# Optimization experiments

Hardware: AMD Instinct MI355X
Metric: run time of the kernel (lower is better)

The kernel has to match this reference:

```python
import jax, jax.numpy as jnp
import numpy as np

N_NODES = 100000


def _deg_norm(idx, n):
    # inverse-sqrt degree, zero-degree nodes -> 0 (DGL norm='both' convention)
    deg = jax.ops.segment_sum(jnp.ones(idx.shape, jnp.float32), idx, num_segments=n)
    return jnp.where(deg > 0, jax.lax.rsqrt(jnp.maximum(deg, 1.0)), 0.0)


def graph_conv(x, src, dst, W, b, n):
    # symmetric normalization: D_out^{-1/2} on src, D_in^{-1/2} on dst
    norm_src = _deg_norm(src, n)  # [N]
    norm_dst = _deg_norm(dst, n)  # [N]
    h = (x * norm_src[:, None]) @ W          # apply weight first (in >= out)
    msg = h[src]                              # gather [E, out]
    agg = jax.ops.segment_sum(msg, dst, num_segments=n)  # scatter-add [N, out]
    return agg * norm_dst[:, None] + b


def setup_inputs() -> dict:
    key = jax.random.key(0)
    ks = jax.random.split(key, 6)
    x = jax.random.normal(ks[0], (N_NODES, 128), dtype=jnp.float32)
    edge_index = jax.random.randint(ks[1], (2, 1600000), 0, N_NODES, dtype=jnp.int64)
    W1 = jax.random.normal(ks[2], (128, 64), dtype=jnp.float32) * (1.0 / np.sqrt(128))
    b1 = jnp.zeros((64,), jnp.float32)
    W2 = jax.random.normal(ks[3], (64, 32), dtype=jnp.float32) * (1.0 / np.sqrt(64))
    b2 = jnp.zeros((32,), jnp.float32)
    Wl = jax.random.normal(ks[4], (32, 1), dtype=jnp.float32) * (1.0 / np.sqrt(32))
    bl = jnp.zeros((1,), jnp.float32)
    return {"x": x, "edge_index": edge_index, "W1": W1, "b1": b1,
            "W2": W2, "b2": b2, "Wl": Wl, "bl": bl}


def reference(x, edge_index, W1, b1, W2, b2, Wl, bl):
    src, dst = edge_index[0], edge_index[1]
    n = x.shape[0]
    h = graph_conv(x, src, dst, W1, b1, n)
    h = jax.nn.relu(h)
    # dropout(p=0.5) is identity at inference
    h = graph_conv(h, src, dst, W2, b2, n)
    return h @ Wl + bl  # [N, 1]
```

## Files before the change

kernel.cpp:

```cpp
#include <hip/hip_runtime.h>
#include <hip/hip_fp16.h>


#define WAVE 64
#define NRANGE 8

typedef _Float16 f16x8 __attribute__((ext_vector_type(8)));
typedef float f32x4 __attribute__((ext_vector_type(4)));

__global__ __launch_bounds__(256) void k_hist(const int* __restrict__ srcArr,
                                              const int* __restrict__ dstArr,
                                              unsigned* __restrict__ partial_s,
                                              unsigned* __restrict__ partial_d,
                                              int E, int B, int C, int chunkE) {
    extern __shared__ unsigned hist[];
    const int r = blockIdx.x & (NRANGE - 1);
    const int c = blockIdx.x >> 3;
    const int lo = r * B;
    const int* nodes = blockIdx.y ? dstArr : srcArr;
    unsigned* partial = blockIdx.y ? partial_d : partial_s;

    for (int b = threadIdx.x; b < B; b += 256) hist[b] = 0u;
    __syncthreads();

    const int beg = c * chunkE, end = min(beg + chunkE, E);
    const int n4 = (end - beg) >> 2;
    const int4* p = (const int4*)(nodes + beg);
    for (int j = threadIdx.x; j < n4; j += 256) {
        int4 v = p[j];
        int a;
        a = v.x - lo; if ((unsigned)a < (unsigned)B) atomicAdd(&hist[a], 1u);
        a = v.y - lo; if ((unsigned)a < (unsigned)B) atomicAdd(&hist[a], 1u);
        a = v.z - lo; if ((unsigned)a < (unsigned)B) atomicAdd(&hist[a], 1u);
        a = v.w - lo; if ((unsigned)a < (unsigned)B) atomicAdd(&hist[a], 1u);
    }
    for (int j = beg + (n4 << 2) + threadIdx.x; j < end; j += 256) {
        int a = nodes[j] - lo;
        if ((unsigned)a < (unsigned)B) atomicAdd(&hist[a], 1u);
    }
    __syncthreads();
    unsigned* outp = partial + (size_t)(r * C + c) * B;
    for (int b = threadIdx.x; b < B; b += 256) outp[b] = hist[b];
}

__global__ __launch_bounds__(256) void k_reduce_norm(const unsigned* __restrict__ partial_s,
                                                     unsigned* __restrict__ partial_d,
                                                     float* __restrict__ norm_s,
                                                     float* __restrict__ norm_d,
                                                     unsigned* __restrict__ deg_d,
                                                     int N, int B, int C) {
    int i = blockIdx.x * 256 + threadIdx.x;
    if (i >= N) return;
    int r = i / B, b = i - r * B;
    size_t base = (size_t)r * C * B + b;
    unsigned ds = 0;
    for (int c = 0; c < C; ++c) ds += partial_s[base + (size_t)c * B];
    unsigned dd = 0;
    for (int c = 0; c < C; ++c) {
        size_t ix = base + (size_t)c * B;
        unsigned v = partial_d[ix];
        partial_d[ix] = dd;
        dd += v;
    }
    deg_d[i] = dd;
    norm_s[i] = ds ? rsqrtf((float)ds) : 0.0f;
    norm_d[i] = dd ? rsqrtf((float)dd) : 0.0f;
}

__global__ void k_w2l(const float* __restrict__ W2, const float* __restrict__ b2,
                      const float* __restrict__ Wl, const float* __restrict__ bl,
                      float* __restrict__ w2l, float* __restrict__ c0) {
    int c = threadIdx.x;
    float acc = 0.f;
#pragma unroll
    for (int j = 0; j < 32; ++j) acc += W2[c * 32 + j] * Wl[j];
    w2l[c] = acc;
    if (c == 0) {
        float s = 0.f;
#pragma unroll
        for (int j = 0; j < 32; ++j) s += b2[j] * Wl[j];
        *c0 = s + bl[0];
    }
}

__global__ __launch_bounds__(256) void k_wt(const float* __restrict__ W1,
                                            _Float16* __restrict__ wt) {
    int t = threadIdx.x;
    for (int i = 0; i < 32; ++i) {
        int e = i * 256 + t;
        int k = e >> 6, n = e & 63;
        wt[n * 128 + k] = (_Float16)W1[e];
    }
}

__global__ __launch_bounds__(256) void k_blocksum(const unsigned* __restrict__ deg,
                                                  unsigned* __restrict__ partial, int N) {
    __shared__ unsigned sw[4];
    int i = blockIdx.x * 256 + threadIdx.x;
    unsigned v = (i < N) ? deg[i] : 0u;
#pragma unroll
    for (int off = 32; off; off >>= 1) v += __shfl_xor((int)v, off);
    if ((threadIdx.x & 63) == 0) sw[threadIdx.x >> 6] = v;
    __syncthreads();
    if (threadIdx.x == 0) partial[blockIdx.x] = sw[0] + sw[1] + sw[2] + sw[3];
}

__global__ __launch_bounds__(512) void k_scanpartial(const unsigned* __restrict__ partial,
                                                     unsigned* __restrict__ blockoff,
                                                     unsigned* __restrict__ offsets,
                                                     int nb, int N) {
    __shared__ unsigned s[512];
    int t = threadIdx.x;
    unsigned v = (t < nb) ? partial[t] : 0u;
    s[t] = v;
    __syncthreads();
    for (int off = 1; off < 512; off <<= 1) {
        unsigned a = (t >= off) ? s[t - off] : 0u;
        __syncthreads();
        s[t] += a;
        __syncthreads();
    }
    if (t < nb) blockoff[t] = s[t] - v;
    if (t == nb - 1) offsets[N] = s[t];
}

__global__ __launch_bounds__(256) void k_offsets(const unsigned* __restrict__ deg,
                                                 const unsigned* __restrict__ blockoff,
                                                 unsigned* __restrict__ offsets, int N) {
    __shared__ unsigned s[256];
    int t = threadIdx.x;
    int i = blockIdx.x * 256 + t;
    unsigned v = (i < N) ? deg[i] : 0u;
    s[t] = v;
    __syncthreads();
    for (int off = 1; off < 256; off <<= 1) {
        unsigned a = (t >= off) ? s[t - off] : 0u;
        __syncthreads();
        s[t] += a;
        __syncthreads();
    }
    if (i < N) offsets[i] = blockoff[blockIdx.x] + s[t] - v;
}

__global__ __launch_bounds__(256) void k_fill(const int* __restrict__ src,
                                              const int* __restrict__ dst,
                                              const unsigned* __restrict__ offsets,
                                              const unsigned* __restrict__ rel,
                                              unsigned* __restrict__ csr,
                                              int N, int E, int B, int C, int chunkE) {
    extern __shared__ unsigned curs[];
    const int r = blockIdx.x & (NRANGE - 1);
    const int c = blockIdx.x >> 3;
    const int lo = r * B;
    const int bins = min(B, N - lo);
    const unsigned* relp = rel + (size_t)(r * C + c) * B;
    for (int b = threadIdx.x; b < bins; b += 256)
        curs[b] = offsets[lo + b] + relp[b];
    __syncthreads();

    const int beg = c * chunkE, end = min(beg + chunkE, E);
    const int n4 = (end - beg) >> 2;
    const int4* pd = (const int4*)(dst + beg);
    const int4* ps = (const int4*)(src + beg);
    for (int j = threadIdx.x; j < n4; j += 256) {
        int4 d4 = pd[j];
        int4 s4 = ps[j];
        int a;
        a = d4.x - lo; if ((unsigned)a < (unsigned)bins) csr[atomicAdd(&curs[a], 1u)] = (unsigned)s4.x;
        a = d4.y - lo; if ((unsigned)a < (unsigned)bins) csr[atomicAdd(&curs[a], 1u)] = (unsigned)s4.y;
        a = d4.z - lo; if ((unsigned)a < (unsigned)bins) csr[atomicAdd(&curs[a], 1u)] = (unsigned)s4.z;
        a = d4.w - lo; if ((unsigned)a < (unsigned)bins) csr[atomicAdd(&curs[a], 1u)] = (unsigned)s4.w;
    }
    for (int j = beg + (n4 << 2) + threadIdx.x; j < end; j += 256) {
        int a = dst[j] - lo;
        if ((unsigned)a < (unsigned)bins) csr[atomicAdd(&curs[a], 1u)] = (unsigned)src[j];
    }
}

__global__ __launch_bounds__(256) void k_gemm1(const float* __restrict__ x,
                                               const _Float16* __restrict__ wt,
                                               const float* __restrict__ norm_s,
                                               __half* __restrict__ h1h, int N) {
    __shared__ __align__(16) _Float16 xs[64 * 128];
    const int tid = threadIdx.x, lane = tid & 63, wv = tid >> 6;
    const int r0 = blockIdx.x * 64;

    f16x8 bf[4][4];
#pragma unroll
    for (int kt = 0; kt < 4; ++kt)
#pragma unroll
        for (int nt = 0; nt < 4; ++nt)
            bf[kt][nt] = *(const f16x8*)&wt[(nt * 16 + (lane & 15)) * 128 +
                                            kt * 32 + (lane >> 4) * 8];

#pragma unroll
    for (int it = 0; it < 8; ++it) {
        int e = it * 256 + tid;
        int r = e >> 5, c = e & 31;
        int row = r0 + r;
        float4 v = (row < N) ? ((const float4*)x)[(size_t)row * 32 + c]
                             : make_float4(0.f, 0.f, 0.f, 0.f);
        __half2 lo2 = __floats2half2_rn(v.x, v.y);
        __half2 hi2 = __floats2half2_rn(v.z, v.w);
        uint2 pk;
        pk.x = *(unsigned*)&lo2;
        pk.y = *(unsigned*)&hi2;
        int byte = r * 256 + c * 8;
        byte ^= (r & 7) << 4;
        *(uint2*)((char*)xs + byte) = pk;
    }
    __syncthreads();

    f32x4 acc[4] = {};
    const int rloc = wv * 16 + (lane & 15);
#pragma unroll
    for (int kt = 0; kt < 4; ++kt) {
        int byte = rloc * 256 + (kt * 32 + (lane >> 4) * 8) * 2;
        byte ^= (rloc & 7) << 4;
        f16x8 af = *(const f16x8*)((char*)xs + byte);
#pragma unroll
        for (int nt = 0; nt < 4; ++nt)
            acc[nt] = __builtin_amdgcn_mfma_f32_16x16x32_f16(af, bf[kt][nt], acc[nt], 0, 0, 0);
    }

#pragma unroll
    for (int j = 0; j < 4; ++j) {
        int row = r0 + wv * 16 + (lane >> 4) * 4 + j;
        if (row < N) {
            float ns = norm_s[row];
#pragma unroll
            for (int nt = 0; nt < 4; ++nt)
                h1h[(size_t)row * 64 + nt * 16 + (lane & 15)] =
                    __float2half(acc[nt][j] * ns);
        }
    }
}

__global__ __launch_bounds__(256) void k_agg_rdot(const unsigned* __restrict__ offsets,
                                                  const unsigned* __restrict__ csr,
                                                  const __half* __restrict__ h1h,
                                                  const float* __restrict__ norm_s,
                                                  const float* __restrict__ norm_d,
                                                  const float* __restrict__ b1,
                                                  const float* __restrict__ w2l,
                                                  float* __restrict__ s_node, int N) {
    const int lane = threadIdx.x & 63;
    const int slot = lane >> 5;
    const int p = lane & 31;
    const int v = (blockIdx.x * 256 + threadIdx.x) >> 6;
    if (v >= N) return;
    const unsigned beg = offsets[v], end = offsets[v + 1];

    float ax = 0.f, ay = 0.f;
    for (unsigned base = beg; base < end; base += WAVE) {
        const int n = (int)min((unsigned)WAVE, end - base);
        int sv = (lane < n) ? (int)csr[base + lane] : 0;
        int i = 0;
        for (; i + 8 <= n; i += 8) {
            int s0 = __shfl(sv, i + 0 + slot);
            int s1 = __shfl(sv, i + 2 + slot);
            int s2 = __shfl(sv, i + 4 + slot);
            int s3 = __shfl(sv, i + 6 + slot);
            unsigned u0 = *(const unsigned*)&h1h[(size_t)s0 * 64 + 2 * p];
            unsigned u1 = *(const unsigned*)&h1h[(size_t)s1 * 64 + 2 * p];
            unsigned u2 = *(const unsigned*)&h1h[(size_t)s2 * 64 + 2 * p];
            unsigned u3 = *(const unsigned*)&h1h[(size_t)s3 * 64 + 2 * p];
            float2 f0 = __half22float2(*(__half2*)&u0);
            float2 f1 = __half22float2(*(__half2*)&u1);
            float2 f2 = __half22float2(*(__half2*)&u2);
            float2 f3 = __half22float2(*(__half2*)&u3);
            ax += (f0.x + f1.x) + (f2.x + f3.x);
            ay += (f0.y + f1.y) + (f2.y + f3.y);
        }
        for (; i < n; i += 2) {
            int e = i + slot;
            int s = __shfl(sv, min(e, n - 1));
            if (e < n) {
                unsigned u = *(const unsigned*)&h1h[(size_t)s * 64 + 2 * p];
                float2 f = __half22float2(*(__half2*)&u);
                ax += f.x; ay += f.y;
            }
        }
    }
    ax += __shfl_xor(ax, 32);
    ay += __shfl_xor(ay, 32);

    float nd = norm_d[v];
    float t = fmaxf(fmaf(ax, nd, b1[2 * p]), 0.f) * w2l[2 * p]
            + fmaxf(fmaf(ay, nd, b1[2 * p + 1]), 0.f) * w2l[2 * p + 1];
#pragma unroll
    for (int off = 16; off; off >>= 1) t += __shfl_xor(t, off);
    if (lane == 0) s_node[v] = t * norm_s[v];
}

__global__ __launch_bounds__(256) void k_out(const unsigned* __restrict__ offsets,
                                             const unsigned* __restrict__ csr,
                                             const float* __restrict__ s_node,
                                             const float* __restrict__ norm_d,
                                             const float* __restrict__ c0,
                                             float* __restrict__ out, int N) {
    int v = blockIdx.x * 256 + threadIdx.x;
    if (v >= N) return;
    unsigned beg = offsets[v], end = offsets[v + 1];
    float sum = 0.f;
    unsigned j = beg;
    for (; j + 4 <= end; j += 4) {
        float a = s_node[csr[j + 0]], b = s_node[csr[j + 1]];
        float c = s_node[csr[j + 2]], d = s_node[csr[j + 3]];
        sum += a + b + c + d;
    }
    for (; j < end; ++j) sum += s_node[csr[j]];
    out[v] = fmaf(sum, norm_d[v], *c0);
}

extern "C" void kernel_launch(void* const* d_in, const int* in_sizes, int n_in,
                              void* d_out, int out_size, void* d_ws, size_t ws_size,
                              hipStream_t stream) {
    const float* x  = (const float*)d_in[0];
    const int*   ei = (const int*)d_in[1];
    const float* W1 = (const float*)d_in[2];
    const float* b1 = (const float*)d_in[3];
    const float* W2 = (const float*)d_in[4];
    const float* b2 = (const float*)d_in[5];
    const float* Wl = (const float*)d_in[6];
    const float* bl = (const float*)d_in[7];

    const int N = in_sizes[0] / 128;
    const int E = in_sizes[1] / 2;
    const int* src = ei;
    const int* dst = ei + E;
    const int NB = (N + 255) / 256;
    const int B = (N + NRANGE - 1) / NRANGE;

    size_t baseBytes = 0;
    {
        auto pad = [](size_t b) { return (b + 255) & ~(size_t)255; };
        baseBytes = pad((size_t)N * 4) * 3 + pad((size_t)(N + 1) * 4) +
                    pad((size_t)NB * 4) * 2 + pad((size_t)N * 64 * 2) +
                    pad((size_t)E * 4) + pad((size_t)N * 4) + pad(64 * 4) + pad(4) +
                    pad(64 * 128 * 2);
    }
    int C = 32;
    while (C > 4 && baseBytes + 2ull * NRANGE * C * B * 4ull > ws_size) C >>= 1;
    const int chunkE = (((E + C - 1) / C) + 3) & ~3;

    char* w = (char*)d_ws;
    auto alloc = [&](size_t bytes) -> void* {
        void* r = (void*)w;
        w += (bytes + 255) & ~(size_t)255;
        return r;
    };
    float*    norm_s    = (float*)alloc((size_t)N * 4);
    float*    norm_d    = (float*)alloc((size_t)N * 4);
    unsigned* deg_d     = (unsigned*)alloc((size_t)N * 4);
    unsigned* offsets   = (unsigned*)alloc((size_t)(N + 1) * 4);
    unsigned* partial   = (unsigned*)alloc((size_t)NB * 4);
    unsigned* blockoff  = (unsigned*)alloc((size_t)NB * 4);
    __half*   h1h       = (__half*)alloc((size_t)N * 64 * 2);
    unsigned* csr       = (unsigned*)alloc((size_t)E * 4);
    float*    s_node    = (float*)alloc((size_t)N * 4);
    float*    w2l       = (float*)alloc(64 * 4);
    float*    c0        = (float*)alloc(4);
    _Float16* wt        = (_Float16*)alloc(64 * 128 * 2);
    unsigned* partial_s = (unsigned*)alloc((size_t)NRANGE * C * B * 4);
    unsigned* partial_d = (unsigned*)alloc((size_t)NRANGE * C * B * 4);

    float* out = (float*)d_out;
    const size_t ldsB = (size_t)B * 4;

    k_hist<<<dim3(NRANGE * C, 2), 256, ldsB, stream>>>(src, dst, partial_s, partial_d,
                                                       E, B, C, chunkE);
    k_w2l<<<1, 64, 0, stream>>>(W2, b2, Wl, bl, w2l, c0);
    k_wt<<<1, 256, 0, stream>>>(W1, wt);
    k_reduce_norm<<<NB, 256, 0, stream>>>(partial_s, partial_d, norm_s, norm_d,
                                          deg_d, N, B, C);

    k_blocksum<<<NB, 256, 0, stream>>>(deg_d, partial, N);
    k_scanpartial<<<1, 512, 0, stream>>>(partial, blockoff, offsets, NB, N);
    k_offsets<<<NB, 256, 0, stream>>>(deg_d, blockoff, offsets, N);

    k_fill<<<NRANGE * C, 256, ldsB, stream>>>(src, dst, offsets, partial_d, csr,
                                              N, E, B, C, chunkE);

    k_gemm1<<<(N + 63) / 64, 256, 0, stream>>>(x, wt, norm_s, h1h, N);

    k_agg_rdot<<<(N + 3) / 4, 256, 0, stream>>>(offsets, csr, h1h, norm_s, norm_d,
                                                b1, w2l, s_node, N);
    k_out<<<NB, 256, 0, stream>>>(offsets, csr, s_node, norm_d, c0, out, N);
}
```

Baseline: 196.3 us.

## Pack two node ranges per LDS histogram word with 16-bit counters

Histogram and fill kernels now pack two node-range bins into one 32-bit LDS word, using the low and high 16 bits. This halves the number of range passes over the edge arrays (4 pairs instead of 8 ranges) and halves the partial-count storage. The fill kernel now computes each CSR slot from the global offset plus a packed per-chunk relative count plus an LDS rank, replacing the preloaded cursors. The aggregation loop also drops the wave-wide shuffle staging and loads CSR indices directly. The 16-bit fields risk overflow if any per-chunk or total node degree reaches 65536.

```diff
diff --git a/kernel.cpp b/kernel.cpp
--- a/kernel.cpp
+++ b/kernel.cpp
@@ -4,6 +4,7 @@
 
 #define WAVE 64
 #define NRANGE 8
+#define NPAIR 4
 
 typedef _Float16 f16x8 __attribute__((ext_vector_type(8)));
 typedef float f32x4 __attribute__((ext_vector_type(4)));
@@ -14,9 +15,9 @@
                                               unsigned* __restrict__ partial_d,
                                               int E, int B, int C, int chunkE) {
     extern __shared__ unsigned hist[];
-    const int r = blockIdx.x & (NRANGE - 1);
-    const int c = blockIdx.x >> 3;
-    const int lo = r * B;
+    const int pr = blockIdx.x & (NPAIR - 1);
+    const int c = blockIdx.x >> 2;
+    const int lo = pr * 2 * B;
     const int* nodes = blockIdx.y ? dstArr : srcArr;
     unsigned* partial = blockIdx.y ? partial_d : partial_s;
 
@@ -29,17 +30,17 @@
     for (int j = threadIdx.x; j < n4; j += 256) {
         int4 v = p[j];
         int a;
-        a = v.x - lo; if ((unsigned)a < (unsigned)B) atomicAdd(&hist[a], 1u);
-        a = v.y - lo; if ((unsigned)a < (unsigned)B) atomicAdd(&hist[a], 1u);
-        a = v.z - lo; if ((unsigned)a < (unsigned)B) atomicAdd(&hist[a], 1u);
-        a = v.w - lo; if ((unsigned)a < (unsigned)B) atomicAdd(&hist[a], 1u);
+        a = v.x - lo; if ((unsigned)a < (unsigned)(2 * B)) { int h = a >= B; atomicAdd(&hist[a - (h ? B : 0)], h ? 0x10000u : 1u); }
+        a = v.y - lo; if ((unsigned)a < (unsigned)(2 * B)) { int h = a >= B; atomicAdd(&hist[a - (h ? B : 0)], h ? 0x10000u : 1u); }
+        a = v.z - lo; if ((unsigned)a < (unsigned)(2 * B)) { int h = a >= B; atomicAdd(&hist[a - (h ? B : 0)], h ? 0x10000u : 1u); }
+        a = v.w - lo; if ((unsigned)a < (unsigned)(2 * B)) { int h = a >= B; atomicAdd(&hist[a - (h ? B : 0)], h ? 0x10000u : 1u); }
     }
     for (int j = beg + (n4 << 2) + threadIdx.x; j < end; j += 256) {
         int a = nodes[j] - lo;
-        if ((unsigned)a < (unsigned)B) atomicAdd(&hist[a], 1u);
-    }
-    __syncthreads();
-    unsigned* outp = partial + (size_t)(r * C + c) * B;
+        if ((unsigned)a < (unsigned)(2 * B)) { int h = a >= B; atomicAdd(&hist[a - (h ? B : 0)], h ? 0x10000u : 1u); }
+    }
+    __syncthreads();
+    unsigned* outp = partial + (size_t)(pr * C + c) * B;
     for (int b = threadIdx.x; b < B; b += 256) outp[b] = hist[b];
 }
 
@@ -49,22 +50,32 @@
                                                      float* __restrict__ norm_d,
                                                      unsigned* __restrict__ deg_d,
                                                      int N, int B, int C) {
-    int i = blockIdx.x * 256 + threadIdx.x;
-    if (i >= N) return;
-    int r = i / B, b = i - r * B;
-    size_t base = (size_t)r * C * B + b;
+    int t = blockIdx.x * 256 + threadIdx.x;
+    if (t >= NPAIR * B) return;
+    int pr = t / B, b = t - pr * B;
+    int n0 = pr * 2 * B + b, n1 = n0 + B;
+    size_t base = (size_t)(pr * C) * B + b;
     unsigned ds = 0;
     for (int c = 0; c < C; ++c) ds += partial_s[base + (size_t)c * B];
-    unsigned dd = 0;
+    unsigned run = 0;
     for (int c = 0; c < C; ++c) {
         size_t ix = base + (size_t)c * B;
         unsigned v = partial_d[ix];
-        partial_d[ix] = dd;
-        dd += v;
-    }
-    deg_d[i] = dd;
-    norm_s[i] = ds ? rsqrtf((float)ds) : 0.0f;
-    norm_d[i] = dd ? rsqrtf((float)dd) : 0.0f;
+        partial_d[ix] = run;
+        run += v;
+    }
+    unsigned ds0 = ds & 0xffffu, ds1 = ds >> 16;
+    unsigned dd0 = run & 0xffffu, dd1 = run >> 16;
+    if (n0 < N) {
+        deg_d[n0] = dd0;
+        norm_s[n0] = ds0 ? rsqrtf((float)ds0) : 0.0f;
+        norm_d[n0] = dd0 ? rsqrtf((float)dd0) : 0.0f;
+    }
+    if (n1 < N) {
+        deg_d[n1] = dd1;
+        norm_s[n1] = ds1 ? rsqrtf((float)ds1) : 0.0f;
+        norm_d[n1] = dd1 ? rsqrtf((float)dd1) : 0.0f;
+    }
 }
 
 __global__ void k_w2l(const float* __restrict__ W2, const float* __restrict__ b2,
@@ -147,16 +158,14 @@
                                               const unsigned* __restrict__ offsets,
                                               const unsigned* __restrict__ rel,
                                               unsigned* __restrict__ csr,
-                                              int N, int E, int B, int C, int chunkE) {
-    extern __shared__ unsigned curs[];
-    const int r = blockIdx.x & (NRANGE - 1);
-    const int c = blockIdx.x >> 3;
-    const int lo = r * B;
-    const int bins = min(B, N - lo);
-    const unsigned* relp = rel + (size_t)(r * C + c) * B;
-    for (int b = threadIdx.x; b < bins; b += 256)
-        curs[b] = offsets[lo + b] + relp[b];
-    __syncthreads();
+                                              int E, int B, int C, int chunkE) {
+    extern __shared__ unsigned rank[];
+    const int pr = blockIdx.x & (NPAIR - 1);
+    const int c = blockIdx.x >> 2;
+    const int lo = pr * 2 * B;
+    for (int b = threadIdx.x; b < B; b += 256) rank[b] = 0u;
+    __syncthreads();
+    const unsigned* relp = rel + (size_t)(pr * C + c) * B;
 
     const int beg = c * chunkE, end = min(beg + chunkE, E);
     const int n4 = (end - beg) >> 2;
@@ -165,15 +174,31 @@
     for (int j = threadIdx.x; j < n4; j += 256) {
         int4 d4 = pd[j];
         int4 s4 = ps[j];
-        int a;
-        a = d4.x - lo; if ((unsigned)a < (unsigned)bins) csr[atomicAdd(&curs[a], 1u)] = (unsigned)s4.x;
-        a = d4.y - lo; if ((unsigned)a < (unsigned)bins) csr[atomicAdd(&curs[a], 1u)] = (unsigned)s4.y;
-        a = d4.z - lo; if ((unsigned)a < (unsigned)bins) csr[atomicAdd(&curs[a], 1u)] = (unsigned)s4.z;
-        a = d4.w - lo; if ((unsigned)a < (unsigned)bins) csr[atomicAdd(&curs[a], 1u)] = (unsigned)s4.w;
+#pragma unroll
+        for (int q = 0; q < 4; ++q) {
+            int d = (&d4.x)[q];
+            int a = d - lo;
+            if ((unsigned)a < (unsigned)(2 * B)) {
+                int h = a >= B;
+                int bin = a - (h ? B : 0);
+                unsigned old = atomicAdd(&rank[bin], h ? 0x10000u : 1u);
+                unsigned rk = (old >> (h ? 16 : 0)) & 0xffffu;
+                unsigned base = offsets[d] + ((relp[bin] >> (h ? 16 : 0)) & 0xffffu);
+                csr[base + rk] = (unsigned)(&s4.x)[q];
+            }
+        }
     }
     for (int j = beg + (n4 << 2) + threadIdx.x; j < end; j += 256) {
-        int a = dst[j] - lo;
-        if ((unsigned)a < (unsigned)bins) csr[atomicAdd(&curs[a], 1u)] = (unsigned)src[j];
+        int d = dst[j];
+        int a = d - lo;
+        if ((unsigned)a < (unsigned)(2 * B)) {
+            int h = a >= B;
+            int bin = a - (h ? B : 0);
+            unsigned old = atomicAdd(&rank[bin], h ? 0x10000u : 1u);
+            unsigned rk = (old >> (h ? 16 : 0)) & 0xffffu;
+            unsigned base = offsets[d] + ((relp[bin] >> (h ? 16 : 0)) & 0xffffu);
+            csr[base + rk] = (unsigned)src[j];
+        }
     }
 }
 
@@ -252,34 +277,30 @@
     const unsigned beg = offsets[v], end = offsets[v + 1];
 
     float ax = 0.f, ay = 0.f;
-    for (unsigned base = beg; base < end; base += WAVE) {
-        const int n = (int)min((unsigned)WAVE, end - base);
-        int sv = (lane < n) ? (int)csr[base + lane] : 0;
-        int i = 0;
-        for (; i + 8 <= n; i += 8) {
-            int s0 = __shfl(sv, i + 0 + slot);
-            int s1 = __shfl(sv, i + 2 + slot);
-            int s2 = __shfl(sv, i + 4 + slot);
-            int s3 = __shfl(sv, i + 6 + slot);
-            unsigned u0 = *(const unsigned*)&h1h[(size_t)s0 * 64 + 2 * p];
-            unsigned u1 = *(const unsigned*)&h1h[(size_t)s1 * 64 + 2 * p];
-            unsigned u2 = *(const unsigned*)&h1h[(size_t)s2 * 64 + 2 * p];
-            unsigned u3 = *(const unsigned*)&h1h[(size_t)s3 * 64 + 2 * p];
-            float2 f0 = __half22float2(*(__half2*)&u0);
-            float2 f1 = __half22float2(*(__half2*)&u1);
-            float2 f2 = __half22float2(*(__half2*)&u2);
-            float2 f3 = __half22float2(*(__half2*)&u3);
-            ax += (f0.x + f1.x) + (f2.x + f3.x);
-            ay += (f0.y + f1.y) + (f2.y + f3.y);
-        }
-        for (; i < n; i += 2) {
-            int e = i + slot;
-            int s = __shfl(sv, min(e, n - 1));
-            if (e < n) {
-                unsigned u = *(const unsigned*)&h1h[(size_t)s * 64 + 2 * p];
-                float2 f = __half22float2(*(__half2*)&u);
-                ax += f.x; ay += f.y;
-            }
+    unsigned i = beg;
+    for (; i + 8 <= end; i += 8) {
+        int s0 = (int)csr[i + 0 + slot];
+        int s1 = (int)csr[i + 2 + slot];
+        int s2 = (int)csr[i + 4 + slot];
+        int s3 = (int)csr[i + 6 + slot];
+        unsigned u0 = *(const unsigned*)&h1h[(size_t)s0 * 64 + 2 * p];
+        unsigned u1 = *(const unsigned*)&h1h[(size_t)s1 * 64 + 2 * p];
+        unsigned u2 = *(const unsigned*)&h1h[(size_t)s2 * 64 + 2 * p];
+        unsigned u3 = *(const unsigned*)&h1h[(size_t)s3 * 64 + 2 * p];
+        float2 f0 = __half22float2(*(__half2*)&u0);
+        float2 f1 = __half22float2(*(__half2*)&u1);
+        float2 f2 = __half22float2(*(__half2*)&u2);
+        float2 f3 = __half22float2(*(__half2*)&u3);
+        ax += (f0.x + f1.x) + (f2.x + f3.x);
+        ay += (f0.y + f1.y) + (f2.y + f3.y);
+    }
+    for (; i < end; i += 2) {
+        unsigned e = i + slot;
+        if (e < end) {
+            int s = (int)csr[e];
+            unsigned u = *(const unsigned*)&h1h[(size_t)s * 64 + 2 * p];
+            float2 f = __half22float2(*(__half2*)&u);
+            ax += f.x; ay += f.y;
         }
     }
     ax += __shfl_xor(ax, 32);
@@ -341,7 +362,7 @@
                     pad(64 * 128 * 2);
     }
     int C = 32;
-    while (C > 4 && baseBytes + 2ull * NRANGE * C * B * 4ull > ws_size) C >>= 1;
+    while (C > 4 && baseBytes + 2ull * NPAIR * C * B * 4ull > ws_size) C >>= 1;
     const int chunkE = (((E + C - 1) / C) + 3) & ~3;
 
     char* w = (char*)d_ws;
@@ -362,25 +383,26 @@
     float*    w2l       = (float*)alloc(64 * 4);
     float*    c0        = (float*)alloc(4);
     _Float16* wt        = (_Float16*)alloc(64 * 128 * 2);
-    unsigned* partial_s = (unsigned*)alloc((size_t)NRANGE * C * B * 4);
-    unsigned* partial_d = (unsigned*)alloc((size_t)NRANGE * C * B * 4);
+    unsigned* partial_s = (unsigned*)alloc((size_t)NPAIR * C * B * 4);
+    unsigned* partial_d = (unsigned*)alloc((size_t)NPAIR * C * B * 4);
 
     float* out = (float*)d_out;
     const size_t ldsB = (size_t)B * 4;
 
-    k_hist<<<dim3(NRANGE * C, 2), 256, ldsB, stream>>>(src, dst, partial_s, partial_d,
-                                                       E, B, C, chunkE);
+    k_hist<<<dim3(NPAIR * C, 2), 256, ldsB, stream>>>(src, dst, partial_s, partial_d,
+                                                      E, B, C, chunkE);
     k_w2l<<<1, 64, 0, stream>>>(W2, b2, Wl, bl, w2l, c0);
     k_wt<<<1, 256, 0, stream>>>(W1, wt);
-    k_reduce_norm<<<NB, 256, 0, stream>>>(partial_s, partial_d, norm_s, norm_d,
-                                          deg_d, N, B, C);
+    k_reduce_norm<<<(NPAIR * B + 255) / 256, 256, 0, stream>>>(partial_s, partial_d,
+                                                               norm_s, norm_d,
+                                                               deg_d, N, B, C);
 
     k_blocksum<<<NB, 256, 0, stream>>>(deg_d, partial, N);
     k_scanpartial<<<1, 512, 0, stream>>>(partial, blockoff, offsets, NB, N);
     k_offsets<<<NB, 256, 0, stream>>>(deg_d, blockoff, offsets, N);
 
-    k_fill<<<NRANGE * C, 256, ldsB, stream>>>(src, dst, offsets, partial_d, csr,
-                                              N, E, B, C, chunkE);
+    k_fill<<<NPAIR * C, 256, ldsB, stream>>>(src, dst, offsets, partial_d, csr,
+                                             E, B, C, chunkE);
 
     k_gemm1<<<(N + 63) / 64, 256, 0, stream>>>(x, wt, norm_s, h1h, N);
 
```

Measured after the change: 236.9 us. 20.7% more time.
